# Kernel tuning notes

Measured on AMD Instinct MI355X. Metric: run time of the kernel, lower is better.

## Reference

```python
import jax, jax.numpy as jnp
import numpy as np

HID, INTER, DK = 768, 1536, 128
NEG_INF = 1.0e12
LOG512 = float(np.log(512.0))


def setup_inputs() -> dict:
    key = jax.random.key(0)
    k1, k2, k3 = jax.random.split(key, 3)
    B, S = 4, 2048
    hidden_states = jax.random.normal(k1, (B, S, HID), dtype=jnp.float32)
    attention_mask = jnp.ones((B, S), dtype=jnp.int32)
    # i_dense: hidden -> 2*INTER + DK (no bias); o_dense: INTER -> hidden (no bias)
    Wi = jax.random.normal(k2, (HID, 2 * INTER + DK), dtype=jnp.float32) * (HID ** -0.5)
    Wo = jax.random.normal(k3, (INTER, HID), dtype=jnp.float32) * (INTER ** -0.5)
    q_gamma = jnp.ones((DK,), dtype=jnp.float32)  # ScaleOffset scale, offset=False
    k_gamma = jnp.ones((DK,), dtype=jnp.float32)
    return {"hidden_states": hidden_states, "Wi": Wi, "Wo": Wo,
            "q_gamma": q_gamma, "k_gamma": k_gamma,
            "attention_mask": attention_mask}


def reference(hidden_states, Wi, Wo, q_gamma, k_gamma, attention_mask):
    # i_dense + swish, then split into u, v, qk
    x = jax.nn.silu(jnp.einsum('bsh,ho->bso', hidden_states, Wi))
    u = x[..., :INTER]
    v = x[..., INTER:2 * INTER]
    qk = x[..., 2 * INTER:]
    q = qk * q_gamma
    k = qk * k_gamma
    # single-head attention scores
    a = jnp.einsum('bmd,bnd->bmn', q, k) / (DK ** 0.5)
    mask = attention_mask[:, None, :]  # [B,1,N]
    a = jnp.where(mask == 0, -NEG_INF, a)
    l = jnp.sum(attention_mask, axis=-1, keepdims=True)[:, :, None].astype(a.dtype)  # [B,1,1]
    # softmax_plus: softmax(a * log(l) / log(512))
    A = jax.nn.softmax(a * jnp.log(l) / LOG512, axis=-1)
    # dropout inactive in eval mode
    o = jnp.einsum('bmi,ih->bmh', u * jnp.einsum('bmn,bnd->bmd', A, v), Wo)
    return o
```

## Files before the change

### kernel.cpp

```cpp
#include <hip/hip_runtime.h>
#include <hip/hip_bf16.h>
#include <math.h>

#define BATCH 4
#define SEQ   2048
#define HID   768
#define INTER 1536
#define DK    128
#define NTOT  3200
#define MROWS 8192
#define LN512 6.2383246250395075f

typedef _Float16 half8  __attribute__((ext_vector_type(8)));
typedef float    floatx4 __attribute__((ext_vector_type(4)));

typedef const __attribute__((address_space(1))) unsigned int* gas1_t;
typedef __attribute__((address_space(3))) unsigned int* las3_t;

static __device__ __forceinline__ void load16(const _Float16* g, _Float16* l) {
    __builtin_amdgcn_global_load_lds((gas1_t)g, (las3_t)l, 16, 0, 0);
}
#define WAIT_VM(N)  asm volatile("s_waitcnt vmcnt(" #N ")" ::: "memory")
#define BARRIER_RAW() asm volatile("s_barrier" ::: "memory")

__global__ void cast_h_kernel(const float* __restrict__ in, _Float16* __restrict__ out, int n) {
    int i = blockIdx.x * blockDim.x + threadIdx.x;
    if (i < n) out[i] = (_Float16)in[i];
}

__global__ void trans_wi_kernel(const float* __restrict__ Wi, _Float16* __restrict__ WiT) {
    int i = blockIdx.x * blockDim.x + threadIdx.x;
    if (i < HID * NTOT) {
        int r = i / NTOT, c = i - r * NTOT;
        WiT[c * HID + r] = (_Float16)Wi[i];
    }
}

__global__ void trans_wo_kernel(const float* __restrict__ Wo, _Float16* __restrict__ WoT) {
    int i = blockIdx.x * blockDim.x + threadIdx.x;
    if (i < INTER * HID) {
        int r = i / HID, c = i - r * HID;
        WoT[c * INTER + r] = (_Float16)Wo[i];
    }
}

__global__ void mask_scales_kernel(const int* __restrict__ mask, float* __restrict__ scales) {
    __shared__ int sh[256];
    int b = blockIdx.x;
    int s = 0;
    for (int i = threadIdx.x; i < SEQ; i += 256) s += mask[b * SEQ + i];
    sh[threadIdx.x] = s;
    __syncthreads();
    for (int off = 128; off > 0; off >>= 1) {
        if (threadIdx.x < off) sh[threadIdx.x] += sh[threadIdx.x + off];
        __syncthreads();
    }
    if (threadIdx.x == 0) scales[b] = logf((float)sh[0]) / LN512;
}

struct TileCtx {
    int tid, wave, lane, quad, l16, wm, wn, c0, c1;
};
static __device__ __forceinline__ TileCtx make_ctx() {
    TileCtx t;
    t.tid = threadIdx.x;
    t.wave = t.tid >> 6; t.lane = t.tid & 63;
    t.quad = t.lane >> 4; t.l16 = t.lane & 15;
    t.wm = (t.wave & 1) * 64;
    t.wn = (t.wave >> 1) * 64;
    t.c0 = t.tid;
    t.c1 = t.tid + 256;
    return t;
}

static __device__ __forceinline__ void gemm_mainloop_db(
    const TileCtx& t,
    const _Float16* __restrict__ Ag, int lda,
    const _Float16* __restrict__ Bg, int ldb,
    int K, _Float16* smem, floatx4 acc[4][4])
{
    const int ar0 = t.c0 >> 2, ak0 = (t.c0 & 3) * 8;
    const int ar1 = t.c1 >> 2, ak1 = (t.c1 & 3) * 8;
    const _Float16* a0 = Ag + (size_t)ar0 * lda + ak0;
    const _Float16* a1 = Ag + (size_t)ar1 * lda + ak1;
    const _Float16* b0 = Bg + (size_t)ar0 * ldb + ak0;
    const _Float16* b1 = Bg + (size_t)ar1 * ldb + ak1;
    _Float16* Asl = smem + t.c0 * 8;
    _Float16* Bsl = smem + 8192 + t.c0 * 8;

    load16(a0, Asl);
    load16(a1, Asl + 2048);
    load16(b0, Bsl);
    load16(b1, Bsl + 2048);

    int buf = 0;
    for (int k0 = 0; k0 < K; k0 += 32) {
        if (k0 + 32 < K) {
            const int nb = (buf ^ 1) * 4096;
            load16(a0 + k0 + 32, Asl + nb);
            load16(a1 + k0 + 32, Asl + nb + 2048);
            load16(b0 + k0 + 32, Bsl + nb);
            load16(b1 + k0 + 32, Bsl + nb + 2048);
            WAIT_VM(4);
        } else {
            WAIT_VM(0);
        }
        BARRIER_RAW();
        const _Float16* Ab = smem + buf * 4096;
        const _Float16* Bb = smem + 8192 + buf * 4096;
        half8 af[4], bf[4];
#pragma unroll
        for (int mt = 0; mt < 4; ++mt)
            af[mt] = *reinterpret_cast<const half8*>(Ab + (t.wm + mt * 16 + t.l16) * 32 + t.quad * 8);
#pragma unroll
        for (int nt = 0; nt < 4; ++nt)
            bf[nt] = *reinterpret_cast<const half8*>(Bb + (t.wn + nt * 16 + t.l16) * 32 + t.quad * 8);
#pragma unroll
        for (int mt = 0; mt < 4; ++mt)
#pragma unroll
            for (int nt = 0; nt < 4; ++nt)
                acc[mt][nt] = __builtin_amdgcn_mfma_f32_16x16x32_f16(af[mt], bf[nt], acc[mt][nt], 0, 0, 0);
        BARRIER_RAW();
        buf ^= 1;
    }
}

__global__ __launch_bounds__(256) void gemm1_kernel(
    const _Float16* __restrict__ Hb, const _Float16* __restrict__ WiT,
    const float* __restrict__ qg, const float* __restrict__ kg,
    _Float16* __restrict__ u, _Float16* __restrict__ vT,
    _Float16* __restrict__ q, _Float16* __restrict__ k)
{
    __shared__ _Float16 smem[16384];
    TileCtx t = make_ctx();
    const int m0 = blockIdx.y * 128;
    const int n0 = blockIdx.x * 128;

    floatx4 acc[4][4] = {};
    gemm_mainloop_db(t, Hb + (size_t)m0 * HID, HID, WiT + (size_t)n0 * HID, HID, HID, smem, acc);

    if (n0 >= INTER && n0 < 2 * INTER) {
        const int bb = m0 >> 11, sloc = m0 & (SEQ - 1), cI = n0 - INTER;
#pragma unroll
        for (int mt = 0; mt < 4; ++mt) {
#pragma unroll
            for (int nt = 0; nt < 4; ++nt) {
                int c = t.wn + nt * 16 + t.l16;
#pragma unroll
                for (int i = 0; i < 4; ++i) {
                    int r = t.wm + mt * 16 + t.quad * 4 + i;
                    float x = acc[mt][nt][i];
                    float y = x / (1.0f + __expf(-x));
                    smem[c * 128 + (r ^ ((c & 15) << 3))] = (_Float16)y;
                }
            }
        }
        __syncthreads();
#pragma unroll
        for (int p = 0; p < 8; ++p) {
            int chunk = t.tid + p * 256;
            int cl = chunk >> 4, sc = chunk & 15;
            int scs = sc ^ (cl & 15);
            half8 v = *reinterpret_cast<const half8*>(smem + cl * 128 + scs * 8);
            *reinterpret_cast<half8*>(vT + ((size_t)bb * INTER + cI + cl) * SEQ + sloc + sc * 8) = v;
        }
    } else {
#pragma unroll
        for (int mt = 0; mt < 4; ++mt) {
#pragma unroll
            for (int nt = 0; nt < 4; ++nt) {
                int col = n0 + t.wn + nt * 16 + t.l16;
#pragma unroll
                for (int i = 0; i < 4; ++i) {
                    int row = m0 + t.wm + mt * 16 + t.quad * 4 + i;
                    float x = acc[mt][nt][i];
                    float y = x / (1.0f + __expf(-x));
                    if (n0 < INTER) {
                        u[(size_t)row * INTER + col] = (_Float16)y;
                    } else {
                        int c = col - 2 * INTER;
                        q[(size_t)row * DK + c] = (_Float16)(y * qg[c]);
                        k[(size_t)row * DK + c] = (_Float16)(y * kg[c]);
                    }
                }
            }
        }
    }
}

__global__ __launch_bounds__(256) void scores_kernel(
    const _Float16* __restrict__ q, const _Float16* __restrict__ k,
    const int* __restrict__ mask, const float* __restrict__ scales,
    _Float16* __restrict__ P)
{
    const int b = blockIdx.y;
    const int m0 = blockIdx.x * 16;
    const int tid = threadIdx.x;
    const int wave = tid >> 6, lane = tid & 63, quad = lane >> 4, l16 = lane & 15;
    const float scale = scales[b];

    half8 aq[4];
    const _Float16* qrow = q + (b * SEQ + m0 + l16) * DK + quad * 8;
#pragma unroll
    for (int kk = 0; kk < 4; ++kk) aq[kk] = *reinterpret_cast<const half8*>(qrow + kk * 32);

    floatx4 sc[32];
#pragma unroll
    for (int nt = 0; nt < 32; ++nt) {
        int n0 = nt * 64 + wave * 16;
        const _Float16* krow = k + (b * SEQ + n0 + l16) * DK + quad * 8;
        floatx4 acc = {};
#pragma unroll
        for (int kk = 0; kk < 4; ++kk) {
            half8 bq = *reinterpret_cast<const half8*>(krow + kk * 32);
            acc = __builtin_amdgcn_mfma_f32_16x16x32_f16(aq[kk], bq, acc, 0, 0, 0);
        }
        sc[nt] = acc;
    }

    const float rs = 0.08838834764831845f * scale;
    const float mval = -1e12f * scale;
    float rmax[4] = {-3.4e38f, -3.4e38f, -3.4e38f, -3.4e38f};
#pragma unroll
    for (int nt = 0; nt < 32; ++nt) {
        int ncol = nt * 64 + wave * 16 + l16;
        bool mok = mask[b * SEQ + ncol] != 0;
#pragma unroll
        for (int i = 0; i < 4; ++i) {
            float s = mok ? sc[nt][i] * rs : mval;
            sc[nt][i] = s;
            rmax[i] = fmaxf(rmax[i], s);
        }
    }
#pragma unroll
    for (int i = 0; i < 4; ++i) {
#pragma unroll
        for (int off = 1; off < 16; off <<= 1)
            rmax[i] = fmaxf(rmax[i], __shfl_xor(rmax[i], off, 64));
    }
    __shared__ float redmax[4][16];
    __shared__ float redsum[4][16];
    if (l16 == 0) {
#pragma unroll
        for (int i = 0; i < 4; ++i) redmax[wave][quad * 4 + i] = rmax[i];
    }
    __syncthreads();
#pragma unroll
    for (int i = 0; i < 4; ++i) {
        int r = quad * 4 + i;
        rmax[i] = fmaxf(fmaxf(redmax[0][r], redmax[1][r]), fmaxf(redmax[2][r], redmax[3][r]));
    }
    float rsum[4] = {0.f, 0.f, 0.f, 0.f};
#pragma unroll
    for (int nt = 0; nt < 32; ++nt) {
#pragma unroll
        for (int i = 0; i < 4; ++i) {
            float e = __expf(sc[nt][i] - rmax[i]);
            sc[nt][i] = e;
            rsum[i] += e;
        }
    }
#pragma unroll
    for (int i = 0; i < 4; ++i) {
#pragma unroll
        for (int off = 1; off < 16; off <<= 1) rsum[i] += __shfl_xor(rsum[i], off, 64);
    }
    if (l16 == 0) {
#pragma unroll
        for (int i = 0; i < 4; ++i) redsum[wave][quad * 4 + i] = rsum[i];
    }
    __syncthreads();
#pragma unroll
    for (int i = 0; i < 4; ++i) {
        int r = quad * 4 + i;
        float tot = redsum[0][r] + redsum[1][r] + redsum[2][r] + redsum[3][r];
        float inv = 1.0f / tot;
        int row = m0 + r;
        _Float16* Prow = P + ((size_t)b * SEQ + row) * SEQ;
#pragma unroll
        for (int nt = 0; nt < 32; ++nt) {
            int ncol = nt * 64 + wave * 16 + l16;
            Prow[ncol] = (_Float16)(sc[nt][i] * inv);
        }
    }
}

__global__ __launch_bounds__(256) void pv_kernel(
    const _Float16* __restrict__ P, const _Float16* __restrict__ vT,
    _Float16* __restrict__ u)
{
    __shared__ _Float16 smem[16384];
    TileCtx t = make_ctx();
    const int b = blockIdx.z;
    const int m0 = blockIdx.y * 128;
    const int n0 = blockIdx.x * 128;
    const _Float16* Pb  = P  + (size_t)b * SEQ * SEQ;
    const _Float16* vTb = vT + (size_t)b * INTER * SEQ;

    floatx4 acc[4][4] = {};
    gemm_mainloop_db(t, Pb + (size_t)m0 * SEQ, SEQ, vTb + (size_t)n0 * SEQ, SEQ, SEQ, smem, acc);

#pragma unroll
    for (int mt = 0; mt < 4; ++mt) {
#pragma unroll
        for (int nt = 0; nt < 4; ++nt) {
            int col = n0 + t.wn + nt * 16 + t.l16;
#pragma unroll
            for (int i = 0; i < 4; ++i) {
                int row = m0 + t.wm + mt * 16 + t.quad * 4 + i;
                size_t gidx = ((size_t)(b * SEQ + row)) * INTER + col;
                float uv = (float)u[gidx];
                u[gidx] = (_Float16)(acc[mt][nt][i] * uv);
            }
        }
    }
}

__global__ __launch_bounds__(256) void gemm2_kernel(
    const _Float16* __restrict__ tin, const _Float16* __restrict__ WoT,
    float* __restrict__ out)
{
    __shared__ _Float16 smem[16384];
    TileCtx t = make_ctx();
    const int m0 = blockIdx.y * 128;
    const int n0 = blockIdx.x * 128;

    floatx4 acc[4][4] = {};
    gemm_mainloop_db(t, tin + (size_t)m0 * INTER, INTER, WoT + (size_t)n0 * INTER, INTER, INTER, smem, acc);

#pragma unroll
    for (int mt = 0; mt < 4; ++mt) {
#pragma unroll
        for (int nt = 0; nt < 4; ++nt) {
            int col = n0 + t.wn + nt * 16 + t.l16;
#pragma unroll
            for (int i = 0; i < 4; ++i) {
                int row = m0 + t.wm + mt * 16 + t.quad * 4 + i;
                out[(size_t)row * HID + col] = acc[mt][nt][i];
            }
        }
    }
}

extern "C" void kernel_launch(void* const* d_in, const int* in_sizes, int n_in,
                              void* d_out, int out_size, void* d_ws, size_t ws_size,
                              hipStream_t stream) {
    const float* H    = (const float*)d_in[0];
    const float* Wi   = (const float*)d_in[1];
    const float* Wo   = (const float*)d_in[2];
    const float* qg   = (const float*)d_in[3];
    const float* kg   = (const float*)d_in[4];
    const int*   mask = (const int*)d_in[5];
    float* out = (float*)d_out;

    char* base = (char*)d_ws;
    size_t off = 0;
    auto alloc = [&](size_t bytes) { void* p = base + off; off = (off + bytes + 255) & ~(size_t)255; return p; };
    _Float16* Hb   = (_Float16*)alloc((size_t)MROWS * HID * 2);
    _Float16* WiT  = (_Float16*)alloc((size_t)NTOT * HID * 2);
    _Float16* WoT  = (_Float16*)alloc((size_t)HID * INTER * 2);
    _Float16* u    = (_Float16*)alloc((size_t)MROWS * INTER * 2);
    _Float16* vT   = (_Float16*)alloc((size_t)BATCH * INTER * SEQ * 2);
    _Float16* q    = (_Float16*)alloc((size_t)MROWS * DK * 2);
    _Float16* k    = (_Float16*)alloc((size_t)MROWS * DK * 2);
    _Float16* P    = (_Float16*)alloc((size_t)BATCH * SEQ * SEQ * 2);
    float*    scales = (float*)alloc(4 * sizeof(float));

    {
        int n = MROWS * HID;
        cast_h_kernel<<<(n + 255) / 256, 256, 0, stream>>>(H, Hb, n);
        trans_wi_kernel<<<(HID * NTOT + 255) / 256, 256, 0, stream>>>(Wi, WiT);
        trans_wo_kernel<<<(INTER * HID + 255) / 256, 256, 0, stream>>>(Wo, WoT);
        mask_scales_kernel<<<BATCH, 256, 0, stream>>>(mask, scales);
    }
    {
        dim3 grid(NTOT / 128, MROWS / 128);
        gemm1_kernel<<<grid, 256, 0, stream>>>(Hb, WiT, qg, kg, u, vT, q, k);
    }
    {
        dim3 grid(SEQ / 16, BATCH);
        scores_kernel<<<grid, 256, 0, stream>>>(q, k, mask, scales, P);
    }
    {
        dim3 grid(INTER / 128, SEQ / 128, BATCH);
        pv_kernel<<<grid, 256, 0, stream>>>(P, vT, u);
    }
    {
        dim3 grid(HID / 128, MROWS / 128);
        gemm2_kernel<<<grid, 256, 0, stream>>>(u, WoT, out);
    }
}
```

Before: 359.5 us.

## Vectorize casts, tile weight transposes, remap GEMM blocks per XCD, add LDS wait

The fp32-to-fp16 cast of the hidden states now handles eight elements per thread with vector loads and stores. Both weight transposes now go through a padded 32x32 shared-memory tile, so global reads and writes are coalesced instead of strided. The three GEMM kernels move to a 1D grid with a swizzled block-to-tile mapping, so blocks landing on the same XCD share rows of A and get better L2 reuse. An explicit lgkmcnt wait is added before the barrier in the main loop, which is a correctness safeguard and may cost a little.

```diff
diff --git a/kernel.cpp b/kernel.cpp
--- a/kernel.cpp
+++ b/kernel.cpp
@@ -20,28 +20,45 @@
 static __device__ __forceinline__ void load16(const _Float16* g, _Float16* l) {
     __builtin_amdgcn_global_load_lds((gas1_t)g, (las3_t)l, 16, 0, 0);
 }
-#define WAIT_VM(N)  asm volatile("s_waitcnt vmcnt(" #N ")" ::: "memory")
+#define WAIT_VM(N)    asm volatile("s_waitcnt vmcnt(" #N ")" ::: "memory")
+#define WAIT_LGKM0()  asm volatile("s_waitcnt lgkmcnt(0)" ::: "memory")
 #define BARRIER_RAW() asm volatile("s_barrier" ::: "memory")
 
 __global__ void cast_h_kernel(const float* __restrict__ in, _Float16* __restrict__ out, int n) {
-    int i = blockIdx.x * blockDim.x + threadIdx.x;
-    if (i < n) out[i] = (_Float16)in[i];
+    int i = (blockIdx.x * blockDim.x + threadIdx.x) * 8;
+    if (i < n) {
+        float4 a = *reinterpret_cast<const float4*>(in + i);
+        float4 b = *reinterpret_cast<const float4*>(in + i + 4);
+        half8 h = {(_Float16)a.x, (_Float16)a.y, (_Float16)a.z, (_Float16)a.w,
+                   (_Float16)b.x, (_Float16)b.y, (_Float16)b.z, (_Float16)b.w};
+        *reinterpret_cast<half8*>(out + i) = h;
+    }
 }
 
 __global__ void trans_wi_kernel(const float* __restrict__ Wi, _Float16* __restrict__ WiT) {
-    int i = blockIdx.x * blockDim.x + threadIdx.x;
-    if (i < HID * NTOT) {
-        int r = i / NTOT, c = i - r * NTOT;
-        WiT[c * HID + r] = (_Float16)Wi[i];
-    }
+    __shared__ _Float16 tile[32][33];
+    const int c0 = blockIdx.x * 32, r0 = blockIdx.y * 32;
+    const int tx = threadIdx.x, ty = threadIdx.y;
+#pragma unroll
+    for (int j = 0; j < 32; j += 8)
+        tile[tx][ty + j] = (_Float16)Wi[(size_t)(r0 + ty + j) * NTOT + c0 + tx];
+    __syncthreads();
+#pragma unroll
+    for (int j = 0; j < 32; j += 8)
+        WiT[(size_t)(c0 + ty + j) * HID + r0 + tx] = tile[ty + j][tx];
 }
 
 __global__ void trans_wo_kernel(const float* __restrict__ Wo, _Float16* __restrict__ WoT) {
-    int i = blockIdx.x * blockDim.x + threadIdx.x;
-    if (i < INTER * HID) {
-        int r = i / HID, c = i - r * HID;
-        WoT[c * INTER + r] = (_Float16)Wo[i];
-    }
+    __shared__ _Float16 tile[32][33];
+    const int c0 = blockIdx.x * 32, r0 = blockIdx.y * 32;
+    const int tx = threadIdx.x, ty = threadIdx.y;
+#pragma unroll
+    for (int j = 0; j < 32; j += 8)
+        tile[tx][ty + j] = (_Float16)Wo[(size_t)(r0 + ty + j) * HID + c0 + tx];
+    __syncthreads();
+#pragma unroll
+    for (int j = 0; j < 32; j += 8)
+        WoT[(size_t)(c0 + ty + j) * INTER + r0 + tx] = tile[ty + j][tx];
 }
 
 __global__ void mask_scales_kernel(const int* __restrict__ mask, float* __restrict__ scales) {
@@ -120,6 +137,7 @@
 #pragma unroll
             for (int nt = 0; nt < 4; ++nt)
                 acc[mt][nt] = __builtin_amdgcn_mfma_f32_16x16x32_f16(af[mt], bf[nt], acc[mt][nt], 0, 0, 0);
+        WAIT_LGKM0();
         BARRIER_RAW();
         buf ^= 1;
     }
@@ -133,8 +151,10 @@
 {
     __shared__ _Float16 smem[16384];
     TileCtx t = make_ctx();
-    const int m0 = blockIdx.y * 128;
-    const int n0 = blockIdx.x * 128;
+    const int f = blockIdx.x;
+    const int xcd = f & 7, i = f >> 3;
+    const int m0 = ((xcd << 3) | (i & 7)) * 128;
+    const int n0 = (i >> 3) * 128;
 
     floatx4 acc[4][4] = {};
     gemm_mainloop_db(t, Hb + (size_t)m0 * HID, HID, WiT + (size_t)n0 * HID, HID, HID, smem, acc);
@@ -147,9 +167,9 @@
             for (int nt = 0; nt < 4; ++nt) {
                 int c = t.wn + nt * 16 + t.l16;
 #pragma unroll
-                for (int i = 0; i < 4; ++i) {
-                    int r = t.wm + mt * 16 + t.quad * 4 + i;
-                    float x = acc[mt][nt][i];
+                for (int i2 = 0; i2 < 4; ++i2) {
+                    int r = t.wm + mt * 16 + t.quad * 4 + i2;
+                    float x = acc[mt][nt][i2];
                     float y = x / (1.0f + __expf(-x));
                     smem[c * 128 + (r ^ ((c & 15) << 3))] = (_Float16)y;
                 }
@@ -171,9 +191,9 @@
             for (int nt = 0; nt < 4; ++nt) {
                 int col = n0 + t.wn + nt * 16 + t.l16;
 #pragma unroll
-                for (int i = 0; i < 4; ++i) {
-                    int row = m0 + t.wm + mt * 16 + t.quad * 4 + i;
-                    float x = acc[mt][nt][i];
+                for (int i2 = 0; i2 < 4; ++i2) {
+                    int row = m0 + t.wm + mt * 16 + t.quad * 4 + i2;
+                    float x = acc[mt][nt][i2];
                     float y = x / (1.0f + __expf(-x));
                     if (n0 < INTER) {
                         u[(size_t)row * INTER + col] = (_Float16)y;
@@ -291,9 +311,11 @@
 {
     __shared__ _Float16 smem[16384];
     TileCtx t = make_ctx();
-    const int b = blockIdx.z;
-    const int m0 = blockIdx.y * 128;
-    const int n0 = blockIdx.x * 128;
+    const int f = blockIdx.x;
+    const int xcd = f & 7, i = f >> 3;
+    const int b = i / 24, j = i % 24;
+    const int m0 = (xcd * 2 + (j & 1)) * 128;
+    const int n0 = (j >> 1) * 128;
     const _Float16* Pb  = P  + (size_t)b * SEQ * SEQ;
     const _Float16* vTb = vT + (size_t)b * INTER * SEQ;
 
@@ -306,11 +328,11 @@
         for (int nt = 0; nt < 4; ++nt) {
             int col = n0 + t.wn + nt * 16 + t.l16;
 #pragma unroll
-            for (int i = 0; i < 4; ++i) {
-                int row = m0 + t.wm + mt * 16 + t.quad * 4 + i;
+            for (int i2 = 0; i2 < 4; ++i2) {
+                int row = m0 + t.wm + mt * 16 + t.quad * 4 + i2;
                 size_t gidx = ((size_t)(b * SEQ + row)) * INTER + col;
                 float uv = (float)u[gidx];
-                u[gidx] = (_Float16)(acc[mt][nt][i] * uv);
+                u[gidx] = (_Float16)(acc[mt][nt][i2] * uv);
             }
         }
     }
@@ -322,8 +344,10 @@
 {
     __shared__ _Float16 smem[16384];
     TileCtx t = make_ctx();
-    const int m0 = blockIdx.y * 128;
-    const int n0 = blockIdx.x * 128;
+    const int f = blockIdx.x;
+    const int xcd = f & 7, i = f >> 3;
+    const int m0 = ((xcd << 3) | (i & 7)) * 128;
+    const int n0 = (i >> 3) * 128;
 
     floatx4 acc[4][4] = {};
     gemm_mainloop_db(t, tin + (size_t)m0 * INTER, INTER, WoT + (size_t)n0 * INTER, INTER, INTER, smem, acc);
@@ -334,9 +358,9 @@
         for (int nt = 0; nt < 4; ++nt) {
             int col = n0 + t.wn + nt * 16 + t.l16;
 #pragma unroll
-            for (int i = 0; i < 4; ++i) {
-                int row = m0 + t.wm + mt * 16 + t.quad * 4 + i;
-                out[(size_t)row * HID + col] = acc[mt][nt][i];
+            for (int i2 = 0; i2 < 4; ++i2) {
+                int row = m0 + t.wm + mt * 16 + t.quad * 4 + i2;
+                out[(size_t)row * HID + col] = acc[mt][nt][i2];
             }
         }
     }
@@ -368,25 +392,16 @@
 
     {
         int n = MROWS * HID;
-        cast_h_kernel<<<(n + 255) / 256, 256, 0, stream>>>(H, Hb, n);
-        trans_wi_kernel<<<(HID * NTOT + 255) / 256, 256, 0, stream>>>(Wi, WiT);
-        trans_wo_kernel<<<(INTER * HID + 255) / 256, 256, 0, stream>>>(Wo, WoT);
+        cast_h_kernel<<<n / 8 / 256, 256, 0, stream>>>(H, Hb, n);
+        trans_wi_kernel<<<dim3(NTOT / 32, HID / 32), dim3(32, 8), 0, stream>>>(Wi, WiT);
+        trans_wo_kernel<<<dim3(HID / 32, INTER / 32), dim3(32, 8), 0, stream>>>(Wo, WoT);
         mask_scales_kernel<<<BATCH, 256, 0, stream>>>(mask, scales);
     }
-    {
-        dim3 grid(NTOT / 128, MROWS / 128);
-        gemm1_kernel<<<grid, 256, 0, stream>>>(Hb, WiT, qg, kg, u, vT, q, k);
-    }
+    gemm1_kernel<<<1600, 256, 0, stream>>>(Hb, WiT, qg, kg, u, vT, q, k);
     {
         dim3 grid(SEQ / 16, BATCH);
         scores_kernel<<<grid, 256, 0, stream>>>(q, k, mask, scales, P);
     }
-    {
-        dim3 grid(INTER / 128, SEQ / 128, BATCH);
-        pv_kernel<<<grid, 256, 0, stream>>>(P, vT, u);
-    }
-    {
-        dim3 grid(HID / 128, MROWS / 128);
-        gemm2_kernel<<<grid, 256, 0, stream>>>(u, WoT, out);
-    }
-}
+    pv_kernel<<<768, 256, 0, stream>>>(P, vT, u);
+    gemm2_kernel<<<384, 256, 0, stream>>>(u, WoT, out);
+}
```

Result: faster. 331.5 us (-7.8%).
